# Kernel optimization log

Hardware: AMD Instinct MI355X
Metric: run time of the kernel (lower is better)

The kernel has to match this reference:

```python
import jax, jax.numpy as jnp
import numpy as np
import math

D_MODEL = 1024
NUM_HEADS = 16
SEQ = 2048
BATCH = 4


def setup_inputs() -> dict:
    key = jax.random.key(0)
    ks = jax.random.split(key, 7)
    s = 0.02
    return {
        "x": jax.random.normal(ks[0], (BATCH, SEQ, D_MODEL), jnp.float32),
        "Wq": jax.random.normal(ks[1], (D_MODEL, D_MODEL), jnp.float32) * s,
        "bq": jax.random.normal(ks[2], (D_MODEL,), jnp.float32) * s,
        "Wkv": jax.random.normal(ks[3], (D_MODEL, 2 * D_MODEL), jnp.float32) * s,
        "bkv": jax.random.normal(ks[4], (2 * D_MODEL,), jnp.float32) * s,
        "Wo": jax.random.normal(ks[5], (D_MODEL, D_MODEL), jnp.float32) * s,
        "bo": jax.random.normal(ks[6], (D_MODEL,), jnp.float32) * s,
        "decoderMask": 1,
    }


def reference(x, Wq, bq, Wkv, bkv, Wo, bo, decoderMask):
    B, S, D = x.shape
    H = NUM_HEADS
    dh = D // H
    q_ = x @ Wq + bq              # [B,S,D]
    kv_ = x @ Wkv + bkv           # [B,S,2D] (self-attention: m is None)
    # Faithful to source: concat [q_, kv_] then reshape into heads of 3*dh,
    # which interleaves Q/KV projection columns across heads.
    qkv = jnp.concatenate([q_, kv_], axis=-1)          # [B,S,3D]
    qkv = qkv.reshape(B, S, H, 3 * dh).transpose(0, 2, 1, 3)  # [B,H,S,3dh]
    q, k, v = jnp.split(qkv, 3, axis=-1)               # each [B,H,S,dh]
    scaled = jnp.einsum("bhqd,bhkd->bhqk", q, k) / math.sqrt(dh)
    if decoderMask:
        mask = jnp.triu(jnp.full((S, S), -jnp.inf, dtype=scaled.dtype), k=1)
        scaled = scaled + mask
    attn = jax.nn.softmax(scaled, axis=-1)
    vals = jnp.einsum("bhqk,bhkd->bhqd", attn, v)      # [B,H,S,dh]
    vals = vals.transpose(0, 2, 1, 3).reshape(B, S, D)
    return vals @ Wo + bo
```

## Files before the change

### kernel.cpp

```cpp
#include <hip/hip_runtime.h>
#include <cstddef>
#include <cstdint>

#define SEQ   2048
#define BATCH 4
#define DM    1024
#define NH    16
#define DH    64
#define ROWS  (BATCH*SEQ)
#define NC3   3072
#define SM_SCALE 0.18033688f

typedef unsigned short u16;
typedef __attribute__((ext_vector_type(8))) short bf16x8;
typedef __attribute__((ext_vector_type(2))) float f32x2;
typedef __attribute__((ext_vector_type(4))) float f32x4;
typedef __attribute__((ext_vector_type(16))) float f32x16;
typedef __attribute__((ext_vector_type(4))) unsigned u32x4;
typedef __attribute__((ext_vector_type(2))) unsigned u32x2;

union V16 { f32x16 v; f32x2 p[8]; };

__device__ __forceinline__ u16 f2b(float f) {
  union { float f; unsigned u; } v; v.f = f;
  unsigned r = v.u + 0x7fffu + ((v.u >> 16) & 1u);
  return (u16)(r >> 16);
}

__device__ __forceinline__ unsigned cvt_pk_bf16(float lo, float hi) {
  unsigned r;
  asm("v_cvt_pk_bf16_f32 %0, %1, %2" : "=v"(r) : "v"(lo), "v"(hi));
  return r;
}

__device__ __forceinline__ void plswap(unsigned& a, unsigned& b) {
  auto rr = __builtin_amdgcn_permlane32_swap((int)a, (int)b, false, false);
  a = (unsigned)rr[0];
  b = (unsigned)rr[1];
}

__device__ __forceinline__ float ex2(float x) { return __builtin_amdgcn_exp2f(x); }

__device__ __forceinline__ void gld16(const void* g, void* l) {
  __builtin_amdgcn_global_load_lds((const __attribute__((address_space(1))) void*)g,
                                   (__attribute__((address_space(3))) void*)l,
                                   16, 0, 0);
}

__global__ __launch_bounds__(256) void prep_tw_kernel(
    const float* __restrict__ x, const float* __restrict__ bq,
    const float* __restrict__ bkv, u16* __restrict__ xb, float* __restrict__ bc,
    const float* __restrict__ Wq, const float* __restrict__ Wkv,
    const float* __restrict__ Wo, u16* __restrict__ Wt)
{
  __shared__ float t_[32][33];
  const int tid = threadIdx.x;
  if (blockIdx.x < 8192) {
    int i = blockIdx.x * 256 + tid;
    int idx = i * 4;
    float4 v = *(const float4*)(x + idx);
    xb[idx + 0] = f2b(v.x);
    xb[idx + 1] = f2b(v.y);
    xb[idx + 2] = f2b(v.z);
    xb[idx + 3] = f2b(v.w);
    if (i < NC3) bc[i] = (i < DM) ? bq[i] : bkv[i - DM];
  } else {
    const int bid = blockIdx.x - 8192;
    const int n0 = (bid & 127) * 32, k0 = (bid >> 7) * 32;
    const int xcol = tid & 31, yrow = tid >> 5;
    #pragma unroll
    for (int it = 0; it < 4; ++it) {
      int k = k0 + yrow + it * 8;
      int n = n0 + xcol;
      float v;
      if (n < DM)           v = Wq[k * DM + n];
      else if (n < NC3)     v = Wkv[k * (2 * DM) + (n - DM)];
      else                  v = Wo[k * DM + (n - NC3)];
      t_[yrow + it * 8][xcol] = v;
    }
    __syncthreads();
    #pragma unroll
    for (int it = 0; it < 4; ++it) {
      int n = n0 + yrow + it * 8;
      int k = k0 + xcol;
      Wt[(size_t)n * DM + k] = f2b(t_[xcol][yrow + it * 8]);
    }
  }
}

__global__ __launch_bounds__(512, 2) void gemm8_qkv(
    const u16* __restrict__ A, const u16* __restrict__ Bt,
    const float* __restrict__ bias, u16* __restrict__ C, u16* __restrict__ Vt)
{
  constexpr int K = 1024, N = NC3;
  constexpr int ASLOT = 16384;
  constexpr int BBASE = 32768;
  constexpr int BSLOT = 12288;
  __shared__ alignas(16) u16 lds_[57344];

  const int tid = threadIdx.x;
  const int lane = tid & 63, wid = tid >> 6;
  const int wr2 = wid >> 2, wc4 = wid & 3;
  const int l15 = lane & 15, lhi = lane >> 4;

  const int bid = blockIdx.x;
  const int xcd = bid & 7, t = bid >> 3;
  const int row0 = (xcd * 4 + (t & 3)) * 256;
  const int hh   = t >> 2;
  const int col0 = hh * 192;

  const int sr = tid >> 3;
  const int scg = ((tid & 7) ^ (sr & 7)) * 8;
  const u16* aSrc = A  + (size_t)(row0 + sr) * K + scg;
  const u16* bSrc = Bt + (size_t)(col0 + sr) * K + scg;
  const int dLin = tid * 8;

  auto stA = [&](int kt, int u) {
    gld16(aSrc + (size_t)(u * 64) * K + kt * 64,
          lds_ + (kt & 1) * ASLOT + u * 4096 + dLin);
  };
  auto stB = [&](int kt, int u) {
    gld16(bSrc + (size_t)(u * 64) * K + kt * 64,
          lds_ + BBASE + (kt & 1) * BSLOT + u * 4096 + dLin);
  };

  int csw[2];
  csw[0] = ((lhi)     ^ (l15 & 7)) * 8;
  csw[1] = ((4 + lhi) ^ (l15 & 7)) * 8;
  const int aBase = wr2 * 8192 + l15 * 64;
  const int bBase = BBASE + (wc4 * 48 + l15) * 64;

  f32x4 acc[8][3];
  #pragma unroll
  for (int m = 0; m < 8; ++m)
    #pragma unroll
    for (int n = 0; n < 3; ++n) { f32x4 z = {0.f, 0.f, 0.f, 0.f}; acc[m][n] = z; }

  stA(0, 0); stA(0, 1); stA(0, 2); stA(0, 3);
  stB(0, 0); stB(0, 1); stB(0, 2);
  stB(1, 0); stB(1, 1); stB(1, 2);
  asm volatile("s_waitcnt vmcnt(3)" ::: "memory");
  __builtin_amdgcn_s_barrier();

  constexpr int KT2 = K / 128;
  for (int j = 0; j < KT2; ++j) {
    const bool last = (j == KT2 - 1);
    #pragma unroll
    for (int hk = 0; hk < 2; ++hk) {
      const int slotA = hk * ASLOT;
      const int slotB = hk * BSLOT;
      bf16x8 bfr[3][2];
      #pragma unroll
      for (int ph = 0; ph < 4; ++ph) {
        const int gp = hk * 4 + ph;
        if (ph == 0) {
          #pragma unroll
          for (int n = 0; n < 3; ++n)
            #pragma unroll
            for (int kk = 0; kk < 2; ++kk)
              bfr[n][kk] = *(const bf16x8*)&lds_[bBase + slotB + n * 1024 + csw[kk]];
        }
        bf16x8 af[2][2];
        #pragma unroll
        for (int mi = 0; mi < 2; ++mi)
          #pragma unroll
          for (int kk = 0; kk < 2; ++kk)
            af[mi][kk] = *(const bf16x8*)&lds_[aBase + slotA + (ph * 2 + mi) * 1024 + csw[kk]];
        switch (gp) {
          case 0: stA(2 * j + 1, 0); stA(2 * j + 1, 1); break;
          case 1: stA(2 * j + 1, 2); stA(2 * j + 1, 3); break;
          case 2: if (!last) { stB(2 * j + 2, 0); stB(2 * j + 2, 1); } break;
          case 3: if (!last) { stB(2 * j + 2, 2); } break;
          case 4: if (!last) { stA(2 * j + 2, 0); stA(2 * j + 2, 1); } break;
          case 5: if (!last) { stA(2 * j + 2, 2); stA(2 * j + 2, 3); } break;
          case 6: if (!last) { stB(2 * j + 3, 0); stB(2 * j + 3, 1); } break;
          case 7: if (!last) { stB(2 * j + 3, 2); } break;
        }
        __builtin_amdgcn_s_barrier();
        asm volatile("s_waitcnt lgkmcnt(0)" ::: "memory");
        __builtin_amdgcn_sched_barrier(0);
        __builtin_amdgcn_s_setprio(1);
        #pragma unroll
        for (int mi = 0; mi < 2; ++mi)
          #pragma unroll
          for (int n = 0; n < 3; ++n) {
            acc[ph * 2 + mi][n] =
                __builtin_amdgcn_mfma_f32_16x16x32_bf16(af[mi][0], bfr[n][0], acc[ph * 2 + mi][n], 0, 0, 0);
            acc[ph * 2 + mi][n] =
                __builtin_amdgcn_mfma_f32_16x16x32_bf16(af[mi][1], bfr[n][1], acc[ph * 2 + mi][n], 0, 0, 0);
          }
        __builtin_amdgcn_s_setprio(0);
        if (gp == 3) {
          if (last) { asm volatile("s_waitcnt vmcnt(0)" ::: "memory"); }
          else      { asm volatile("s_waitcnt vmcnt(3)" ::: "memory"); }
        } else if (gp == 7 && !last) {
          asm volatile("s_waitcnt vmcnt(3)" ::: "memory");
        }
        __builtin_amdgcn_s_barrier();
      }
    }
  }

  #pragma unroll
  for (int m = 0; m < 8; ++m) {
    const int row = row0 + wr2 * 128 + m * 16 + lhi * 4;
    #pragma unroll
    for (int n = 0; n < 3; ++n) {
      const int cc  = wc4 * 48 + n * 16 + l15;
      const int col = col0 + cc;
      const float bv = bias[col];
      if (cc < 128) {
        const float qs = (cc < 64) ? SM_SCALE : 1.f;
        #pragma unroll
        for (int r = 0; r < 4; ++r)
          C[(size_t)(row + r) * N + col] = f2b((acc[m][n][r] + bv) * qs);
      } else {
        u16 wv[4];
        #pragma unroll
        for (int r = 0; r < 4; ++r) wv[r] = f2b(acc[m][n][r] + bv);
        const int bb = row >> 11, jj = row & (SEQ - 1);
        u16* vt = Vt + ((size_t)(bb * NH + hh) * 64 + (cc - 128)) * SEQ + jj;
        u32x2 pv = { (unsigned)wv[0] | ((unsigned)wv[1] << 16),
                     (unsigned)wv[2] | ((unsigned)wv[3] << 16) };
        *(u32x2*)vt = pv;
      }
    }
  }
}

__global__ __launch_bounds__(256) void gemm_out(
    const u16* __restrict__ A, const u16* __restrict__ Bt,
    const float* __restrict__ bias, float* __restrict__ C, int M, int N, int K)
{
  __shared__ alignas(16) u16 lds_[3 * 8192];
  const int tid = threadIdx.x;
  const int lane = tid & 63, wid = tid >> 6;
  const int wr = (wid >> 1) * 64, wc = (wid & 1) * 64;
  const int l15 = lane & 15, lhi = lane >> 4;

  const int bid = blockIdx.x;
  const int xcd = bid & 7, t = bid >> 3;
  const int rsub = t & 7, colb = t >> 3;
  const int row0 = (xcd * 8 + rsub) * 128, col0 = colb * 128;
  const int sr = tid >> 2;
  const int scol = (((tid & 3) ^ ((sr >> 1) & 3)) * 8);

  const u16* aS0 = A  + (size_t)(row0 + sr) * K + scol;
  const u16* aS1 = A  + (size_t)(row0 + 64 + sr) * K + scol;
  const u16* bS0 = Bt + (size_t)(col0 + sr) * K + scol;
  const u16* bS1 = Bt + (size_t)(col0 + 64 + sr) * K + scol;
  const int dA = tid * 8;

  const int csw = ((lhi ^ ((l15 >> 1) & 3)) * 8);
  int aoff[4], boff[4];
  #pragma unroll
  for (int m = 0; m < 4; ++m) aoff[m] = (wr + m * 16 + l15) * 32 + csw;
  #pragma unroll
  for (int n = 0; n < 4; ++n) boff[n] = 4096 + (wc + n * 16 + l15) * 32 + csw;

  f32x4 acc[4][4];
  #pragma unroll
  for (int m = 0; m < 4; ++m)
    #pragma unroll
    for (int n = 0; n < 4; ++n) { f32x4 z = {0.f, 0.f, 0.f, 0.f}; acc[m][n] = z; }

  const int KT = K >> 5;
  auto stage = [&](int kt, u16* base) {
    const int ka = kt * 32;
    gld16(aS0 + ka, base + dA);
    gld16(aS1 + ka, base + 2048 + dA);
    gld16(bS0 + ka, base + 4096 + dA);
    gld16(bS1 + ka, base + 6144 + dA);
  };

  u16* const bufA = lds_;
  u16* const bufB = lds_ + 8192;
  u16* const bufC = lds_ + 16384;

  stage(0, bufA); stage(1, bufB);
  asm volatile("s_waitcnt vmcnt(4)" ::: "memory");
  __builtin_amdgcn_s_barrier();

  u16* rb = bufA;
  u16* sb = bufC;
  for (int kt = 0; kt < KT; ++kt) {
    bf16x8 a[4], b[4];
    #pragma unroll
    for (int m = 0; m < 4; ++m) a[m] = *(const bf16x8*)&rb[aoff[m]];
    #pragma unroll
    for (int n = 0; n < 4; ++n) b[n] = *(const bf16x8*)&rb[boff[n]];
    if (kt + 2 < KT) stage(kt + 2, sb);
    __builtin_amdgcn_s_setprio(1);
    #pragma unroll
    for (int m = 0; m < 4; ++m)
      #pragma unroll
      for (int n = 0; n < 4; ++n)
        acc[m][n] = __builtin_amdgcn_mfma_f32_16x16x32_bf16(a[m], b[n], acc[m][n], 0, 0, 0);
    __builtin_amdgcn_s_setprio(0);
    if (kt + 1 < KT) {
      if (kt + 2 < KT) { asm volatile("s_waitcnt vmcnt(4)" ::: "memory"); }
      else             { asm volatile("s_waitcnt vmcnt(0)" ::: "memory"); }
      __builtin_amdgcn_s_barrier();
    }
    rb = (rb == bufC) ? bufA : rb + 8192;
    sb = (sb == bufC) ? bufA : sb + 8192;
  }

  #pragma unroll
  for (int m = 0; m < 4; ++m)
    #pragma unroll
    for (int n = 0; n < 4; ++n) {
      const int col = col0 + wc + n * 16 + l15;
      const float bv = bias[col];
      #pragma unroll
      for (int r = 0; r < 4; ++r) {
        const int row = row0 + wr + m * 16 + lhi * 4 + r;
        C[(size_t)row * N + col] = acc[m][n][r] + bv;
      }
    }
}

__global__ __launch_bounds__(512, 4) void attn_kernel(
    const u16* __restrict__ qkv, const u16* __restrict__ Vt, u16* __restrict__ ctx)
{
  const int bid = blockIdx.x;
  const int p   = (bid >> 3) & 7;
  const int g   = (bid & 7) + ((bid >> 6) << 3);
  const int h   = g & 15, b = g >> 4;
  const int tid = threadIdx.x;
  const int lane = tid & 63;
  const int hf  = tid >> 8;
  const int wid = (tid >> 6) & 3;
  const int l31 = lane & 31, lhi5 = lane >> 5;

  __shared__ alignas(16) u16 smem_[2 * 16384];
  u16* const smem = smem_ + hf * 16384;

  const int qt  = hf ? (7 - p) : (8 + p);
  const int q0  = qt * 128;
  const int ntL = qt * 2 + 2;
  const int ntMax = (8 + p) * 2 + 2;

  const size_t kv_row = (size_t)(b * NH + h) * 64;
  const int st = tid & 255;
  const int sr = st >> 3, sck = st & 7;
  const int scks = sck ^ (sr & 7);

  const u16* kSrc0 = qkv + (size_t)(b * SEQ + sr) * NC3 + h * 192 + 64 + scks * 8;
  const u16* kSrc1 = kSrc0 + (size_t)32 * NC3;
  const u16* vSrc0 = Vt + (kv_row + sr) * SEQ + scks * 8;
  const u16* vSrc1 = vSrc0 + (size_t)32 * SEQ;
  const int dOff0 = sr * 64 + sck * 8;
  const int dOff1 = (32 + sr) * 64 + sck * 8;

  int koff[4], koff2[4];
  #pragma unroll
  for (int c = 0; c < 4; ++c) {
    koff[c]  = l31 * 64        + (((2 * c + lhi5) ^ (l31 & 7)) * 8);
    koff2[c] = (32 + l31) * 64 + (((2 * c + lhi5) ^ (l31 & 7)) * 8);
  }

  #pragma unroll
  for (int it = 0; it < 4; ++it) {
    int row = it * 32 + sr;
    gld16(qkv + (size_t)(b * SEQ + q0 + row) * NC3 + h * 192 + scks * 8,
          &smem[row * 64 + sck * 8]);
  }
  gld16(kSrc0, &smem[8192 + dOff0]);
  gld16(kSrc1, &smem[8192 + dOff1]);
  gld16(vSrc0, &smem[12288 + dOff0]);
  gld16(vSrc1, &smem[12288 + dOff1]);
  __syncthreads();

  bf16x8 qf[4];
  {
    const int qrow = wid * 32 + l31;
    #pragma unroll
    for (int c = 0; c < 4; ++c)
      qf[c] = *(const bf16x8*)&smem[qrow * 64 + (((2 * c + lhi5) ^ (qrow & 7)) * 8)];
  }
  __syncthreads();

  V16 o0, o1;
  #pragma unroll
  for (int r = 0; r < 16; ++r) { o0.v[r] = 0.f; o1.v[r] = 0.f; }
  float lrow = 0.f;

  const int qw0 = q0 + wid * 32;
  const int qa  = qw0 + l31;
  const int dqb = qa - 4 * lhi5;

  #pragma unroll 1
  for (int jt = 0; jt < ntMax; ++jt) {
    const int j0 = jt * 64;
    const u16* Kb = smem + ((jt & 1) ? 0 : 8192);
    const u16* Vb = smem + ((jt & 1) ? 4096 : 12288);

    if (jt + 1 < ntL) {
      u16* Kn = smem + ((jt & 1) ? 8192 : 0);
      u16* Vn = smem + ((jt & 1) ? 12288 : 4096);
      const size_t kAdv = (size_t)(j0 + 64) * NC3;
      const int    vAdv = j0 + 64;
      gld16(kSrc0 + kAdv, &Kn[dOff0]);
      gld16(kSrc1 + kAdv, &Kn[dOff1]);
      gld16(vSrc0 + vAdv, &Vn[dOff0]);
      gld16(vSrc1 + vAdv, &Vn[dOff1]);
    }

    if (j0 <= qw0 + 31) {
      V16 s0, s1;
      #pragma unroll
      for (int r = 0; r < 16; ++r) { s0.v[r] = 0.f; s1.v[r] = 0.f; }
      __builtin_amdgcn_s_setprio(1);
      #pragma unroll
      for (int c = 0; c < 4; ++c) {
        bf16x8 kf = *(const bf16x8*)&Kb[koff[c]];
        s0.v = __builtin_amdgcn_mfma_f32_32x32x16_bf16(kf, qf[c], s0.v, 0, 0, 0);
      }
      #pragma unroll
      for (int c = 0; c < 4; ++c) {
        bf16x8 kf = *(const bf16x8*)&Kb[koff2[c]];
        s1.v = __builtin_amdgcn_mfma_f32_32x32x16_bf16(kf, qf[c], s1.v, 0, 0, 0);
      }
      __builtin_amdgcn_s_setprio(0);

      if (j0 + 63 > qw0) {
        const int dq = dqb - j0;
        #pragma unroll
        for (int r = 0; r < 16; ++r) {
          const int kvc = (r & 3) + 8 * (r >> 2);
          s0.v[r] = (kvc > dq)      ? -1e30f : s0.v[r];
          s1.v[r] = (kvc + 32 > dq) ? -1e30f : s1.v[r];
        }
      }

      f32x2 sum2 = {0.f, 0.f};
      #pragma unroll
      for (int i = 0; i < 8; ++i) {
        f32x2 e0, e1;
        e0[0] = ex2(s0.p[i][0]); e0[1] = ex2(s0.p[i][1]);
        e1[0] = ex2(s1.p[i][0]); e1[1] = ex2(s1.p[i][1]);
        s0.p[i] = e0; s1.p[i] = e1;
        sum2 += e0 + e1;
      }
      float ps = sum2[0] + sum2[1];
      {
        unsigned a = __builtin_bit_cast(unsigned, ps), bb = a;
        plswap(a, bb);
        ps = __builtin_bit_cast(float, a) + __builtin_bit_cast(float, bb);
      }
      lrow += ps;

      unsigned pk0[8], pk1[8];
      #pragma unroll
      for (int i = 0; i < 4; ++i) {
        pk0[2 * i]     = cvt_pk_bf16(s0.v[4 * i + 0], s0.v[4 * i + 1]);
        pk0[2 * i + 1] = cvt_pk_bf16(s0.v[4 * i + 2], s0.v[4 * i + 3]);
        pk1[2 * i]     = cvt_pk_bf16(s1.v[4 * i + 0], s1.v[4 * i + 1]);
        pk1[2 * i + 1] = cvt_pk_bf16(s1.v[4 * i + 2], s1.v[4 * i + 3]);
      }
      bf16x8 pf[4];
      {
        unsigned a0 = pk0[0], b0 = pk0[2]; plswap(a0, b0);
        unsigned a1 = pk0[1], b1 = pk0[3]; plswap(a1, b1);
        u32x4 w0v = {a0, a1, b0, b1}; pf[0] = __builtin_bit_cast(bf16x8, w0v);
        unsigned a2 = pk0[4], b2 = pk0[6]; plswap(a2, b2);
        unsigned a3 = pk0[5], b3 = pk0[7]; plswap(a3, b3);
        u32x4 w1v = {a2, a3, b2, b3}; pf[1] = __builtin_bit_cast(bf16x8, w1v);
        unsigned a4 = pk1[0], b4 = pk1[2]; plswap(a4, b4);
        unsigned a5 = pk1[1], b5 = pk1[3]; plswap(a5, b5);
        u32x4 w2v = {a4, a5, b4, b5}; pf[2] = __builtin_bit_cast(bf16x8, w2v);
        unsigned a6 = pk1[4], b6 = pk1[6]; plswap(a6, b6);
        unsigned a7 = pk1[5], b7 = pk1[7]; plswap(a7, b7);
        u32x4 w3v = {a6, a7, b6, b7}; pf[3] = __builtin_bit_cast(bf16x8, w3v);
      }

      __builtin_amdgcn_s_setprio(1);
      #pragma unroll
      for (int c = 0; c < 4; ++c) {
        bf16x8 vf = *(const bf16x8*)&Vb[koff[c]];
        o0.v = __builtin_amdgcn_mfma_f32_32x32x16_bf16(vf, pf[c], o0.v, 0, 0, 0);
      }
      #pragma unroll
      for (int c = 0; c < 4; ++c) {
        bf16x8 vf = *(const bf16x8*)&Vb[koff2[c]];
        o1.v = __builtin_amdgcn_mfma_f32_32x32x16_bf16(vf, pf[c], o1.v, 0, 0, 0);
      }
      __builtin_amdgcn_s_setprio(0);
    }
    __syncthreads();
  }

  const float inv = 1.f / lrow;
  u16* crow = ctx + (size_t)(b * SEQ + qa) * DM + h * DH;
  #pragma unroll
  for (int i = 0; i < 4; ++i) {
    u32x2 v0, v1;
    v0[0] = cvt_pk_bf16(o0.v[4 * i + 0] * inv, o0.v[4 * i + 1] * inv);
    v0[1] = cvt_pk_bf16(o0.v[4 * i + 2] * inv, o0.v[4 * i + 3] * inv);
    v1[0] = cvt_pk_bf16(o1.v[4 * i + 0] * inv, o1.v[4 * i + 1] * inv);
    v1[1] = cvt_pk_bf16(o1.v[4 * i + 2] * inv, o1.v[4 * i + 3] * inv);
    *(u32x2*)&crow[8 * i + 4 * lhi5]      = v0;
    *(u32x2*)&crow[32 + 8 * i + 4 * lhi5] = v1;
  }
}

extern "C" void kernel_launch(void* const* d_in, const int* in_sizes, int n_in,
                              void* d_out, int out_size, void* d_ws, size_t ws_size,
                              hipStream_t stream) {
  (void)in_sizes; (void)n_in; (void)out_size; (void)ws_size;
  const float* x   = (const float*)d_in[0];
  const float* Wq  = (const float*)d_in[1];
  const float* bq  = (const float*)d_in[2];
  const float* Wkv = (const float*)d_in[3];
  const float* bkv = (const float*)d_in[4];
  const float* Wo  = (const float*)d_in[5];
  const float* bo  = (const float*)d_in[6];
  float* out = (float*)d_out;

  char* w = (char*)d_ws;
  size_t off = 0;
  auto alloc = [&](size_t bytes) { void* p = w + off; off += (bytes + 255) & ~(size_t)255; return p; };
  u16*   xb   = (u16*)alloc((size_t)ROWS * DM * 2);
  u16*   qkvb = (u16*)alloc((size_t)ROWS * NC3 * 2);
  u16*   Vt   = (u16*)alloc((size_t)BATCH * NH * DH * SEQ * 2);
  u16*   Wt   = (u16*)alloc((size_t)4096 * DM * 2);
  float* bc   = (float*)alloc((size_t)NC3 * 4);
  u16*   ctx  = xb;

  prep_tw_kernel<<<dim3(8192 + 4096), 256, 0, stream>>>(x, bq, bkv, xb, bc, Wq, Wkv, Wo, Wt);
  gemm8_qkv<<<dim3(512), 512, 0, stream>>>(xb, Wt, bc, qkvb, Vt);
  attn_kernel<<<dim3(512), 512, 0, stream>>>(qkvb, Vt, ctx);
  gemm_out<<<dim3(512), 256, 0, stream>>>(ctx, Wt + (size_t)NC3 * DM, bo, out, ROWS, DM, DM);
}
```

Baseline: 156.5 us.

## Rewrite output projection GEMM with 256x128 tiles, 8 waves and phased prefetch

Replaces the 128x128-tile, 4-wave output GEMM with a 256x128-tile, 8-wave kernel that stages K in 64-wide chunks. A and B loads are double-buffered in LDS and interleaved with the MFMA phases under explicit barriers and waitcnts. The larger tile raises arithmetic intensity and roughly halves global traffic per FLOP, and the grid drops to 256 blocks. With fewer blocks and many barriers per iteration, the CUs may be underfilled and synchronisation overhead may grow.

```diff
diff --git a/kernel.cpp b/kernel.cpp
--- a/kernel.cpp
+++ b/kernel.cpp
@@ -228,96 +228,129 @@
   }
 }
 
-__global__ __launch_bounds__(256) void gemm_out(
+__global__ __launch_bounds__(512, 2) void gemm8_out(
     const u16* __restrict__ A, const u16* __restrict__ Bt,
-    const float* __restrict__ bias, float* __restrict__ C, int M, int N, int K)
+    const float* __restrict__ bias, float* __restrict__ C)
 {
-  __shared__ alignas(16) u16 lds_[3 * 8192];
+  constexpr int K = 1024, N = DM;
+  constexpr int ASLOT = 16384;
+  constexpr int BBASE = 32768;
+  constexpr int BSLOT = 8192;
+  __shared__ alignas(16) u16 lds_[49152];
+
   const int tid = threadIdx.x;
   const int lane = tid & 63, wid = tid >> 6;
-  const int wr = (wid >> 1) * 64, wc = (wid & 1) * 64;
+  const int wr2 = wid >> 2, wc4 = wid & 3;
   const int l15 = lane & 15, lhi = lane >> 4;
 
   const int bid = blockIdx.x;
   const int xcd = bid & 7, t = bid >> 3;
-  const int rsub = t & 7, colb = t >> 3;
-  const int row0 = (xcd * 8 + rsub) * 128, col0 = colb * 128;
-  const int sr = tid >> 2;
-  const int scol = (((tid & 3) ^ ((sr >> 1) & 3)) * 8);
-
-  const u16* aS0 = A  + (size_t)(row0 + sr) * K + scol;
-  const u16* aS1 = A  + (size_t)(row0 + 64 + sr) * K + scol;
-  const u16* bS0 = Bt + (size_t)(col0 + sr) * K + scol;
-  const u16* bS1 = Bt + (size_t)(col0 + 64 + sr) * K + scol;
-  const int dA = tid * 8;
-
-  const int csw = ((lhi ^ ((l15 >> 1) & 3)) * 8);
-  int aoff[4], boff[4];
-  #pragma unroll
-  for (int m = 0; m < 4; ++m) aoff[m] = (wr + m * 16 + l15) * 32 + csw;
-  #pragma unroll
-  for (int n = 0; n < 4; ++n) boff[n] = 4096 + (wc + n * 16 + l15) * 32 + csw;
-
-  f32x4 acc[4][4];
-  #pragma unroll
-  for (int m = 0; m < 4; ++m)
-    #pragma unroll
-    for (int n = 0; n < 4; ++n) { f32x4 z = {0.f, 0.f, 0.f, 0.f}; acc[m][n] = z; }
-
-  const int KT = K >> 5;
-  auto stage = [&](int kt, u16* base) {
-    const int ka = kt * 32;
-    gld16(aS0 + ka, base + dA);
-    gld16(aS1 + ka, base + 2048 + dA);
-    gld16(bS0 + ka, base + 4096 + dA);
-    gld16(bS1 + ka, base + 6144 + dA);
+  const int row0 = (xcd * 4 + (t & 3)) * 256;
+  const int col0 = (t >> 2) * 128;
+
+  const int sr = tid >> 3;
+  const int scg = ((tid & 7) ^ (sr & 7)) * 8;
+  const u16* aSrc = A  + (size_t)(row0 + sr) * K + scg;
+  const u16* bSrc = Bt + (size_t)(col0 + sr) * K + scg;
+  const int dLin = tid * 8;
+
+  auto stA = [&](int kt, int u) {
+    gld16(aSrc + (size_t)(u * 64) * K + kt * 64,
+          lds_ + (kt & 1) * ASLOT + u * 4096 + dLin);
   };
-
-  u16* const bufA = lds_;
-  u16* const bufB = lds_ + 8192;
-  u16* const bufC = lds_ + 16384;
-
-  stage(0, bufA); stage(1, bufB);
-  asm volatile("s_waitcnt vmcnt(4)" ::: "memory");
+  auto stB = [&](int kt, int u) {
+    gld16(bSrc + (size_t)(u * 64) * K + kt * 64,
+          lds_ + BBASE + (kt & 1) * BSLOT + u * 4096 + dLin);
+  };
+
+  int csw[2];
+  csw[0] = ((lhi)     ^ (l15 & 7)) * 8;
+  csw[1] = ((4 + lhi) ^ (l15 & 7)) * 8;
+  const int aBase = wr2 * 8192 + l15 * 64;
+  const int bBase = BBASE + (wc4 * 32 + l15) * 64;
+
+  f32x4 acc[8][2];
+  #pragma unroll
+  for (int m = 0; m < 8; ++m)
+    #pragma unroll
+    for (int n = 0; n < 2; ++n) { f32x4 z = {0.f, 0.f, 0.f, 0.f}; acc[m][n] = z; }
+
+  stA(0, 0); stA(0, 1); stA(0, 2); stA(0, 3);
+  stB(0, 0); stB(0, 1);
+  stB(1, 0); stB(1, 1);
+  asm volatile("s_waitcnt vmcnt(2)" ::: "memory");
   __builtin_amdgcn_s_barrier();
 
-  u16* rb = bufA;
-  u16* sb = bufC;
-  for (int kt = 0; kt < KT; ++kt) {
-    bf16x8 a[4], b[4];
-    #pragma unroll
-    for (int m = 0; m < 4; ++m) a[m] = *(const bf16x8*)&rb[aoff[m]];
-    #pragma unroll
-    for (int n = 0; n < 4; ++n) b[n] = *(const bf16x8*)&rb[boff[n]];
-    if (kt + 2 < KT) stage(kt + 2, sb);
-    __builtin_amdgcn_s_setprio(1);
-    #pragma unroll
-    for (int m = 0; m < 4; ++m)
-      #pragma unroll
-      for (int n = 0; n < 4; ++n)
-        acc[m][n] = __builtin_amdgcn_mfma_f32_16x16x32_bf16(a[m], b[n], acc[m][n], 0, 0, 0);
-    __builtin_amdgcn_s_setprio(0);
-    if (kt + 1 < KT) {
-      if (kt + 2 < KT) { asm volatile("s_waitcnt vmcnt(4)" ::: "memory"); }
-      else             { asm volatile("s_waitcnt vmcnt(0)" ::: "memory"); }
-      __builtin_amdgcn_s_barrier();
-    }
-    rb = (rb == bufC) ? bufA : rb + 8192;
-    sb = (sb == bufC) ? bufA : sb + 8192;
-  }
-
-  #pragma unroll
-  for (int m = 0; m < 4; ++m)
-    #pragma unroll
-    for (int n = 0; n < 4; ++n) {
-      const int col = col0 + wc + n * 16 + l15;
+  constexpr int KT2 = K / 128;
+  for (int j = 0; j < KT2; ++j) {
+    const bool last = (j == KT2 - 1);
+    #pragma unroll
+    for (int hk = 0; hk < 2; ++hk) {
+      const int slotA = hk * ASLOT;
+      const int slotB = hk * BSLOT;
+      bf16x8 bfr[2][2];
+      #pragma unroll
+      for (int ph = 0; ph < 4; ++ph) {
+        const int gp = hk * 4 + ph;
+        if (ph == 0) {
+          #pragma unroll
+          for (int n = 0; n < 2; ++n)
+            #pragma unroll
+            for (int kk = 0; kk < 2; ++kk)
+              bfr[n][kk] = *(const bf16x8*)&lds_[bBase + slotB + n * 1024 + csw[kk]];
+        }
+        bf16x8 af[2][2];
+        #pragma unroll
+        for (int mi = 0; mi < 2; ++mi)
+          #pragma unroll
+          for (int kk = 0; kk < 2; ++kk)
+            af[mi][kk] = *(const bf16x8*)&lds_[aBase + slotA + (ph * 2 + mi) * 1024 + csw[kk]];
+        switch (gp) {
+          case 0: stA(2 * j + 1, 0); stA(2 * j + 1, 1); break;
+          case 1: stA(2 * j + 1, 2); stA(2 * j + 1, 3); break;
+          case 2: if (!last) { stB(2 * j + 2, 0); stB(2 * j + 2, 1); } break;
+          case 4: if (!last) { stA(2 * j + 2, 0); stA(2 * j + 2, 1); } break;
+          case 5: if (!last) { stA(2 * j + 2, 2); stA(2 * j + 2, 3); } break;
+          case 6: if (!last) { stB(2 * j + 3, 0); stB(2 * j + 3, 1); } break;
+          default: break;
+        }
+        __builtin_amdgcn_s_barrier();
+        asm volatile("s_waitcnt lgkmcnt(0)" ::: "memory");
+        __builtin_amdgcn_sched_barrier(0);
+        __builtin_amdgcn_s_setprio(1);
+        #pragma unroll
+        for (int mi = 0; mi < 2; ++mi)
+          #pragma unroll
+          for (int n = 0; n < 2; ++n) {
+            acc[ph * 2 + mi][n] =
+                __builtin_amdgcn_mfma_f32_16x16x32_bf16(af[mi][0], bfr[n][0], acc[ph * 2 + mi][n], 0, 0, 0);
+            acc[ph * 2 + mi][n] =
+                __builtin_amdgcn_mfma_f32_16x16x32_bf16(af[mi][1], bfr[n][1], acc[ph * 2 + mi][n], 0, 0, 0);
+          }
+        __builtin_amdgcn_s_setprio(0);
+        if (gp == 3) {
+          if (last) { asm volatile("s_waitcnt vmcnt(0)" ::: "memory"); }
+          else      { asm volatile("s_waitcnt vmcnt(2)" ::: "memory"); }
+        } else if (gp == 7 && !last) {
+          asm volatile("s_waitcnt vmcnt(2)" ::: "memory");
+        }
+        __builtin_amdgcn_s_barrier();
+      }
+    }
+  }
+
+  #pragma unroll
+  for (int m = 0; m < 8; ++m) {
+    const int row = row0 + wr2 * 128 + m * 16 + lhi * 4;
+    #pragma unroll
+    for (int n = 0; n < 2; ++n) {
+      const int col = col0 + wc4 * 32 + n * 16 + l15;
       const float bv = bias[col];
       #pragma unroll
-      for (int r = 0; r < 4; ++r) {
-        const int row = row0 + wr + m * 16 + lhi * 4 + r;
-        C[(size_t)row * N + col] = acc[m][n][r] + bv;
-      }
-    }
+      for (int r = 0; r < 4; ++r)
+        C[(size_t)(row + r) * N + col] = acc[m][n][r] + bv;
+    }
+  }
 }
 
 __global__ __launch_bounds__(512, 4) void attn_kernel(
@@ -531,5 +564,5 @@
   prep_tw_kernel<<<dim3(8192 + 4096), 256, 0, stream>>>(x, bq, bkv, xb, bc, Wq, Wkv, Wo, Wt);
   gemm8_qkv<<<dim3(512), 512, 0, stream>>>(xb, Wt, bc, qkvb, Vt);
   attn_kernel<<<dim3(512), 512, 0, stream>>>(qkvb, Vt, ctx);
-  gemm_out<<<dim3(512), 256, 0, stream>>>(ctx, Wt + (size_t)NC3 * DM, bo, out, ROWS, DM, DM);
-}
+  gemm8_out<<<dim3(256), 512, 0, stream>>>(ctx, Wt + (size_t)NC3 * DM, bo, out);
+}
```

New measurement: 154.1 us. Within noise of the previous version (-1.5%).
